# Optimization experiments

Measured on AMD Instinct MI355X. Metric: run time of the kernel, lower is better.

The kernel has to match this reference:

```python
import jax, jax.numpy as jnp
import numpy as np

N_NODES = 8192


def spmm(edge_src, edge_dst, edge_w, h):
    # out[dst] += w * h[src]  — sparse adjacency @ dense matrix
    msg = h[edge_src] * edge_w[:, None]
    return jax.ops.segment_sum(msg, edge_dst, num_segments=N_NODES)


def setup_inputs() -> dict:
    key = jax.random.key(0)
    k_x, k_s, k_d, k_w, k_w1, k_w2 = jax.random.split(key, 6)
    x = jax.random.normal(k_x, (N_NODES, 512), dtype=jnp.float32)
    edge_src = jax.random.randint(k_s, (262144,), 0, N_NODES, dtype=jnp.int32)
    edge_dst = jax.random.randint(k_d, (262144,), 0, N_NODES, dtype=jnp.int32)
    edge_w = jax.random.uniform(k_w, (262144,), dtype=jnp.float32)
    W1 = jax.random.normal(k_w1, (512, 256), dtype=jnp.float32) * 0.05
    W2 = jax.random.normal(k_w2, (256, 64), dtype=jnp.float32) * 0.05
    return {"x": x, "edge_src": edge_src, "edge_dst": edge_dst,
            "edge_w": edge_w, "W1": W1, "W2": W2}


def reference(x, edge_src, edge_dst, edge_w, W1, W2):
    # GCN layer 1: relu(A @ (X W1))
    h1 = jax.nn.relu(spmm(edge_src, edge_dst, edge_w, x @ W1))
    # GCN layer 2 (linear act): Z = A @ (H1 W2)
    z = spmm(edge_src, edge_dst, edge_w, h1 @ W2)
    # InnerProductDecoder with identity act: Z @ Z^T
    recon = jnp.einsum('nd,md->nm', z, z)
    return recon
```

## Files before the change

### kernel.cpp

```cpp
#include <hip/hip_runtime.h>
#include <hip/hip_bf16.h>

#define NN     8192
#define D0     512
#define D1     256
#define D2     64
#define NE     262144

typedef __attribute__((ext_vector_type(8)))  __bf16 bf16x8;
typedef __attribute__((ext_vector_type(16))) float  f32x16;

__global__ __launch_bounds__(256) void prep_k(const float* __restrict__ X,
                                              const float* __restrict__ W,
                                              int4* __restrict__ zero_region,
                                              __bf16* __restrict__ Xh,
                                              __bf16* __restrict__ Xl,
                                              __bf16* __restrict__ Th,
                                              __bf16* __restrict__ Tl) {
    const int bid = blockIdx.x;
    const int tid = threadIdx.x;
    if (bid < 16) {
        zero_region[bid * 256 + tid] = make_int4(0, 0, 0, 0);
    } else if (bid < 16 + 2048) {
        const int i = (bid - 16) * 256 + tid;
        float4 v0 = reinterpret_cast<const float4*>(X)[i * 2 + 0];
        float4 v1 = reinterpret_cast<const float4*>(X)[i * 2 + 1];
        float f[8] = {v0.x, v0.y, v0.z, v0.w, v1.x, v1.y, v1.z, v1.w};
        bf16x8 h, l;
        #pragma unroll
        for (int j = 0; j < 8; ++j) {
            __bf16 hj = (__bf16)f[j];
            h[j] = hj;
            l[j] = (__bf16)(f[j] - (float)hj);
        }
        reinterpret_cast<bf16x8*>(Xh)[i] = h;
        reinterpret_cast<bf16x8*>(Xl)[i] = l;
    } else {
        __shared__ float t[32][33];
        const int cid = bid - 16 - 2048;
        const int c0 = (cid & 7) * 32;
        const int k0 = (cid >> 3) * 32;
        {
            int tr  = tid >> 3;
            int tc4 = tid & 7;
            float4 v = *reinterpret_cast<const float4*>(&W[(k0 + tr) * D1 + c0 + tc4 * 4]);
            t[tr][tc4 * 4 + 0] = v.x;
            t[tr][tc4 * 4 + 1] = v.y;
            t[tr][tc4 * 4 + 2] = v.z;
            t[tr][tc4 * 4 + 3] = v.w;
        }
        __syncthreads();
        int c  = tid >> 3;
        int kq = (tid & 7) * 4;
        __bf16 hv[4], lv[4];
        #pragma unroll
        for (int j = 0; j < 4; ++j) {
            float f = t[kq + j][c];
            hv[j] = (__bf16)f;
            lv[j] = (__bf16)(f - (float)hv[j]);
        }
        *reinterpret_cast<uint2*>(&Th[(size_t)(c0 + c) * D0 + k0 + kq]) = *reinterpret_cast<uint2*>(hv);
        *reinterpret_cast<uint2*>(&Tl[(size_t)(c0 + c) * D0 + k0 + kq]) = *reinterpret_cast<uint2*>(lv);
    }
}

__global__ __launch_bounds__(256) void gemm1_mfma_k(const __bf16* __restrict__ Xh,
                                                    const __bf16* __restrict__ Xl,
                                                    const __bf16* __restrict__ Wh,
                                                    const __bf16* __restrict__ Wl,
                                                    float* __restrict__ O) {
    const int tid  = threadIdx.x;
    const int lane = tid & 63;
    const int w    = tid >> 6;
    const int wm   = w >> 1;
    const int wn   = w & 1;
    const int r32  = lane & 31;
    const int kh   = lane >> 5;
    const int row  = blockIdx.x * 64 + wm * 32 + r32;
    const int col  = blockIdx.y * 64 + wn * 32 + r32;

    const __bf16* pAh = Xh + (size_t)row * D0;
    const __bf16* pAl = Xl + (size_t)row * D0;
    const __bf16* pBh = Wh + (size_t)col * D0;
    const __bf16* pBl = Wl + (size_t)col * D0;

    f32x16 acc = {};
    #pragma unroll 8
    for (int k0 = 0; k0 < D0; k0 += 16) {
        const int koff = k0 + kh * 8;
        bf16x8 ah = *reinterpret_cast<const bf16x8*>(pAh + koff);
        bf16x8 al = *reinterpret_cast<const bf16x8*>(pAl + koff);
        bf16x8 bh = *reinterpret_cast<const bf16x8*>(pBh + koff);
        bf16x8 bl = *reinterpret_cast<const bf16x8*>(pBl + koff);
        acc = __builtin_amdgcn_mfma_f32_32x32x16_bf16(ah, bh, acc, 0, 0, 0);
        acc = __builtin_amdgcn_mfma_f32_32x32x16_bf16(ah, bl, acc, 0, 0, 0);
        acc = __builtin_amdgcn_mfma_f32_32x32x16_bf16(al, bh, acc, 0, 0, 0);
    }

    const int rowBase = blockIdx.x * 64 + wm * 32;
    const int colBase = blockIdx.y * 64 + wn * 32;
    #pragma unroll
    for (int reg = 0; reg < 16; ++reg) {
        int r = (reg & 3) + 8 * (reg >> 2) + 4 * kh;
        O[(size_t)(rowBase + r) * D1 + colBase + r32] = acc[reg];
    }
}

__global__ __launch_bounds__(256) void hist_k(const int* __restrict__ dst,
                                              int* __restrict__ counts) {
    int i = blockIdx.x * 256 + threadIdx.x;
    if (i < NE) atomicAdd(&counts[dst[i]], 1);
}

__global__ __launch_bounds__(256) void scan_k(const int* __restrict__ counts,
                                              int* __restrict__ rs) {
    __shared__ int wsum[4];
    const int tid  = threadIdx.x;
    const int base = tid * 32;
    int v[32];
    int s = 0;
    #pragma unroll
    for (int j = 0; j < 8; ++j) {
        int4 q = reinterpret_cast<const int4*>(&counts[base])[j];
        v[j * 4 + 0] = q.x; v[j * 4 + 1] = q.y; v[j * 4 + 2] = q.z; v[j * 4 + 3] = q.w;
        s += q.x + q.y + q.z + q.w;
    }
    int inc = s;
    #pragma unroll
    for (int off = 1; off < 64; off <<= 1) {
        int t = __shfl_up(inc, off, 64);
        if ((tid & 63) >= off) inc += t;
    }
    if ((tid & 63) == 63) wsum[tid >> 6] = inc;
    __syncthreads();
    int wpre = 0;
    #pragma unroll
    for (int wi = 0; wi < 4; ++wi) if (wi < (tid >> 6)) wpre += wsum[wi];
    int ex = wpre + inc - s;
    #pragma unroll
    for (int j = 0; j < 32; ++j) { rs[base + j] = ex; ex += v[j]; }
    if (tid == 0) rs[NN] = NE;
}

__global__ __launch_bounds__(256) void scatter_k(const int* __restrict__ src,
                                                 const int* __restrict__ dst,
                                                 const float* __restrict__ w,
                                                 const int* __restrict__ rs,
                                                 int* __restrict__ cursor,
                                                 int* __restrict__ eps,
                                                 float* __restrict__ epw) {
    int i = blockIdx.x * 256 + threadIdx.x;
    if (i < NE) {
        int d = dst[i];
        int pos = rs[d] + atomicAdd(&cursor[d], 1);
        eps[pos] = src[i];
        epw[pos] = w[i];
    }
}

__global__ __launch_bounds__(256) void spmmfuse_k(const float* __restrict__ Hin,
                                                  const int* __restrict__ rs,
                                                  const int* __restrict__ eps,
                                                  const float* __restrict__ epw,
                                                  const float* __restrict__ W2,
                                                  float* __restrict__ H1W2) {
    __shared__ float h1row[D1];
    const int row = blockIdx.x;
    const int tid = threadIdx.x;
    const int start = rs[row], end = rs[row + 1];
    float acc = 0.f;
    for (int j = start; j < end; ++j) {
        acc += epw[j] * Hin[(size_t)eps[j] * D1 + tid];
    }
    h1row[tid] = fmaxf(acc, 0.f);
    __syncthreads();
    if (tid < D2) {
        float o = 0.f;
        #pragma unroll 16
        for (int k = 0; k < D1; ++k) o += h1row[k] * W2[k * D2 + tid];
        H1W2[(size_t)row * D2 + tid] = o;
    }
}

__global__ __launch_bounds__(256) void spmm64_k(const float* __restrict__ Hin,
                                                const int* __restrict__ rs,
                                                const int* __restrict__ eps,
                                                const float* __restrict__ epw,
                                                __bf16* __restrict__ Zh,
                                                __bf16* __restrict__ Zl) {
    const int row = blockIdx.x * 4 + (threadIdx.x >> 6);
    const int c = threadIdx.x & 63;
    const int start = rs[row], end = rs[row + 1];
    float acc = 0.f;
    for (int j = start; j < end; ++j) {
        acc += epw[j] * Hin[eps[j] * D2 + c];
    }
    __bf16 h = (__bf16)acc;
    Zh[row * D2 + c] = h;
    Zl[row * D2 + c] = (__bf16)(acc - (float)h);
}

__global__ __launch_bounds__(256) void zzt_k(const __bf16* __restrict__ Zh,
                                             const __bf16* __restrict__ Zl,
                                             float* __restrict__ O) {
    const int tid  = threadIdx.x;
    const int lane = tid & 63;
    const int w    = tid >> 6;
    const int wm   = w >> 1;
    const int wn   = w & 1;
    const int r32  = lane & 31;
    const int kh   = lane >> 5;
    const int rowBase = blockIdx.y * 128 + wm * 64;
    const int colBase = blockIdx.x * 128 + wn * 64;

    f32x16 acc[2][2] = {};

    #pragma unroll
    for (int kk = 0; kk < 4; ++kk) {
        const int koff = kk * 16 + kh * 8;
        bf16x8 ah0 = *reinterpret_cast<const bf16x8*>(&Zh[(rowBase +      r32) * D2 + koff]);
        bf16x8 ah1 = *reinterpret_cast<const bf16x8*>(&Zh[(rowBase + 32 + r32) * D2 + koff]);
        bf16x8 al0 = *reinterpret_cast<const bf16x8*>(&Zl[(rowBase +      r32) * D2 + koff]);
        bf16x8 al1 = *reinterpret_cast<const bf16x8*>(&Zl[(rowBase + 32 + r32) * D2 + koff]);
        bf16x8 bh0 = *reinterpret_cast<const bf16x8*>(&Zh[(colBase +      r32) * D2 + koff]);
        bf16x8 bh1 = *reinterpret_cast<const bf16x8*>(&Zh[(colBase + 32 + r32) * D2 + koff]);
        bf16x8 bl0 = *reinterpret_cast<const bf16x8*>(&Zl[(colBase +      r32) * D2 + koff]);
        bf16x8 bl1 = *reinterpret_cast<const bf16x8*>(&Zl[(colBase + 32 + r32) * D2 + koff]);

        acc[0][0] = __builtin_amdgcn_mfma_f32_32x32x16_bf16(ah0, bh0, acc[0][0], 0, 0, 0);
        acc[0][1] = __builtin_amdgcn_mfma_f32_32x32x16_bf16(ah0, bh1, acc[0][1], 0, 0, 0);
        acc[1][0] = __builtin_amdgcn_mfma_f32_32x32x16_bf16(ah1, bh0, acc[1][0], 0, 0, 0);
        acc[1][1] = __builtin_amdgcn_mfma_f32_32x32x16_bf16(ah1, bh1, acc[1][1], 0, 0, 0);

        acc[0][0] = __builtin_amdgcn_mfma_f32_32x32x16_bf16(ah0, bl0, acc[0][0], 0, 0, 0);
        acc[0][1] = __builtin_amdgcn_mfma_f32_32x32x16_bf16(ah0, bl1, acc[0][1], 0, 0, 0);
        acc[1][0] = __builtin_amdgcn_mfma_f32_32x32x16_bf16(ah1, bl0, acc[1][0], 0, 0, 0);
        acc[1][1] = __builtin_amdgcn_mfma_f32_32x32x16_bf16(ah1, bl1, acc[1][1], 0, 0, 0);

        acc[0][0] = __builtin_amdgcn_mfma_f32_32x32x16_bf16(al0, bh0, acc[0][0], 0, 0, 0);
        acc[0][1] = __builtin_amdgcn_mfma_f32_32x32x16_bf16(al0, bh1, acc[0][1], 0, 0, 0);
        acc[1][0] = __builtin_amdgcn_mfma_f32_32x32x16_bf16(al1, bh0, acc[1][0], 0, 0, 0);
        acc[1][1] = __builtin_amdgcn_mfma_f32_32x32x16_bf16(al1, bh1, acc[1][1], 0, 0, 0);
    }

    #pragma unroll
    for (int i = 0; i < 2; ++i)
        #pragma unroll
        for (int j = 0; j < 2; ++j)
            #pragma unroll
            for (int reg = 0; reg < 16; ++reg) {
                int r = (reg & 3) + 8 * (reg >> 2) + 4 * kh;
                __builtin_nontemporal_store(acc[i][j][reg],
                    &O[(size_t)(rowBase + i * 32 + r) * NN + colBase + j * 32 + r32]);
            }
}

extern "C" void kernel_launch(void* const* d_in, const int* in_sizes, int n_in,
                              void* d_out, int out_size, void* d_ws, size_t ws_size,
                              hipStream_t stream) {
    const float* x        = (const float*)d_in[0];
    const int*   edge_src = (const int*)d_in[1];
    const int*   edge_dst = (const int*)d_in[2];
    const float* edge_w   = (const float*)d_in[3];
    const float* W1       = (const float*)d_in[4];
    const float* W2       = (const float*)d_in[5];
    float* out = (float*)d_out;

    char* ws = (char*)d_ws;
    const size_t OFF_XW1  = 0;
    const size_t OFF_H1W2 = OFF_XW1  + (size_t)NN * D1 * 4;
    const size_t OFF_ZH   = OFF_H1W2 + (size_t)NN * D2 * 4;
    const size_t OFF_ZL   = OFF_ZH   + (size_t)NN * D2 * 2;
    const size_t OFF_XH   = OFF_ZL   + (size_t)NN * D2 * 2;
    const size_t OFF_XL   = OFF_XH   + (size_t)NN * D0 * 2;
    const size_t OFF_WTH  = OFF_XL   + (size_t)NN * D0 * 2;
    const size_t OFF_WTL  = OFF_WTH  + (size_t)D0 * D1 * 2;
    const size_t OFF_RS   = OFF_WTL  + (size_t)D0 * D1 * 2;
    const size_t OFF_CNT  = OFF_RS   + 33280;
    const size_t OFF_CUR  = OFF_CNT  + (size_t)NN * 4;
    const size_t OFF_EPS  = OFF_CUR  + (size_t)NN * 4;
    const size_t OFF_EPW  = OFF_EPS  + (size_t)NE * 4;

    float*  xw1  = (float*)(ws + OFF_XW1);
    float*  h1w2 = (float*)(ws + OFF_H1W2);
    __bf16* zh   = (__bf16*)(ws + OFF_ZH);
    __bf16* zl   = (__bf16*)(ws + OFF_ZL);
    __bf16* xh   = (__bf16*)(ws + OFF_XH);
    __bf16* xl   = (__bf16*)(ws + OFF_XL);
    __bf16* wth  = (__bf16*)(ws + OFF_WTH);
    __bf16* wtl  = (__bf16*)(ws + OFF_WTL);
    int*    rs   = (int*)(ws + OFF_RS);
    int*    cnt  = (int*)(ws + OFF_CNT);
    int*    eps  = (int*)(ws + OFF_EPS);
    float*  epw  = (float*)(ws + OFF_EPW);
    int*    cur  = (int*)(ws + OFF_CUR);

    prep_k<<<16 + 2048 + 128, 256, 0, stream>>>(x, W1, (int4*)cnt, xh, xl, wth, wtl);

    gemm1_mfma_k<<<dim3(NN / 64, D1 / 64), 256, 0, stream>>>(xh, xl, wth, wtl, xw1);

    hist_k<<<NE / 256, 256, 0, stream>>>(edge_dst, cnt);
    scan_k<<<1, 256, 0, stream>>>(cnt, rs);
    scatter_k<<<NE / 256, 256, 0, stream>>>(edge_src, edge_dst, edge_w, rs, cur, eps, epw);

    spmmfuse_k<<<NN, 256, 0, stream>>>(xw1, rs, eps, epw, W2, h1w2);

    spmm64_k<<<NN / 4, 256, 0, stream>>>(h1w2, rs, eps, epw, zh, zl);

    zzt_k<<<dim3(NN / 128, NN / 128), 256, 0, stream>>>(zh, zl, out);
}
```

Measured before the change: 235.4 us.

## Exploit ZZ^T symmetry, fuse X bf16 split into GEMM1, batch SpMM rows

The Z·Z^T kernel now launches only the upper-triangular 128x128 tiles. Each off-diagonal tile writes its transpose through a padded shared-memory buffer, which roughly halves the MFMA work for the dominant output GEMM. The X hi/lo bf16 split moves from prep_k into a 128x128-tiled gemm1, removing a round trip of X through global memory. hist_k reads int4 destination indices, and spmmfuse_k handles four rows per block with W2 cached in shared memory. Costs include large shared-memory use (about 67 KB in zzt, 64 KB in spmmfuse) that lowers occupancy, and redundant per-k conversion work in gemm1.

```diff
diff --git a/kernel.cpp b/kernel.cpp
--- a/kernel.cpp
+++ b/kernel.cpp
@@ -9,35 +9,19 @@
 
 typedef __attribute__((ext_vector_type(8)))  __bf16 bf16x8;
 typedef __attribute__((ext_vector_type(16))) float  f32x16;
-
-__global__ __launch_bounds__(256) void prep_k(const float* __restrict__ X,
-                                              const float* __restrict__ W,
+typedef __attribute__((ext_vector_type(4)))  float  f32x4;
+
+__global__ __launch_bounds__(256) void prep_k(const float* __restrict__ W,
                                               int4* __restrict__ zero_region,
-                                              __bf16* __restrict__ Xh,
-                                              __bf16* __restrict__ Xl,
                                               __bf16* __restrict__ Th,
                                               __bf16* __restrict__ Tl) {
     const int bid = blockIdx.x;
     const int tid = threadIdx.x;
     if (bid < 16) {
         zero_region[bid * 256 + tid] = make_int4(0, 0, 0, 0);
-    } else if (bid < 16 + 2048) {
-        const int i = (bid - 16) * 256 + tid;
-        float4 v0 = reinterpret_cast<const float4*>(X)[i * 2 + 0];
-        float4 v1 = reinterpret_cast<const float4*>(X)[i * 2 + 1];
-        float f[8] = {v0.x, v0.y, v0.z, v0.w, v1.x, v1.y, v1.z, v1.w};
-        bf16x8 h, l;
-        #pragma unroll
-        for (int j = 0; j < 8; ++j) {
-            __bf16 hj = (__bf16)f[j];
-            h[j] = hj;
-            l[j] = (__bf16)(f[j] - (float)hj);
-        }
-        reinterpret_cast<bf16x8*>(Xh)[i] = h;
-        reinterpret_cast<bf16x8*>(Xl)[i] = l;
     } else {
         __shared__ float t[32][33];
-        const int cid = bid - 16 - 2048;
+        const int cid = bid - 16;
         const int c0 = (cid & 7) * 32;
         const int k0 = (cid >> 3) * 32;
         {
@@ -64,8 +48,7 @@
     }
 }
 
-__global__ __launch_bounds__(256) void gemm1_mfma_k(const __bf16* __restrict__ Xh,
-                                                    const __bf16* __restrict__ Xl,
+__global__ __launch_bounds__(256) void gemm1_mfma_k(const float* __restrict__ X,
                                                     const __bf16* __restrict__ Wh,
                                                     const __bf16* __restrict__ Wl,
                                                     float* __restrict__ O) {
@@ -76,40 +59,62 @@
     const int wn   = w & 1;
     const int r32  = lane & 31;
     const int kh   = lane >> 5;
-    const int row  = blockIdx.x * 64 + wm * 32 + r32;
-    const int col  = blockIdx.y * 64 + wn * 32 + r32;
-
-    const __bf16* pAh = Xh + (size_t)row * D0;
-    const __bf16* pAl = Xl + (size_t)row * D0;
-    const __bf16* pBh = Wh + (size_t)col * D0;
-    const __bf16* pBl = Wl + (size_t)col * D0;
-
-    f32x16 acc = {};
-    #pragma unroll 8
+    const int rowBase = blockIdx.x * 128 + wm * 64;
+    const int colBase = blockIdx.y * 128 + wn * 64;
+
+    f32x16 acc[2][2] = {};
+
     for (int k0 = 0; k0 < D0; k0 += 16) {
         const int koff = k0 + kh * 8;
-        bf16x8 ah = *reinterpret_cast<const bf16x8*>(pAh + koff);
-        bf16x8 al = *reinterpret_cast<const bf16x8*>(pAl + koff);
-        bf16x8 bh = *reinterpret_cast<const bf16x8*>(pBh + koff);
-        bf16x8 bl = *reinterpret_cast<const bf16x8*>(pBl + koff);
-        acc = __builtin_amdgcn_mfma_f32_32x32x16_bf16(ah, bh, acc, 0, 0, 0);
-        acc = __builtin_amdgcn_mfma_f32_32x32x16_bf16(ah, bl, acc, 0, 0, 0);
-        acc = __builtin_amdgcn_mfma_f32_32x32x16_bf16(al, bh, acc, 0, 0, 0);
-    }
-
-    const int rowBase = blockIdx.x * 64 + wm * 32;
-    const int colBase = blockIdx.y * 64 + wn * 32;
-    #pragma unroll
-    for (int reg = 0; reg < 16; ++reg) {
-        int r = (reg & 3) + 8 * (reg >> 2) + 4 * kh;
-        O[(size_t)(rowBase + r) * D1 + colBase + r32] = acc[reg];
-    }
-}
-
-__global__ __launch_bounds__(256) void hist_k(const int* __restrict__ dst,
+        bf16x8 ah[2], al[2];
+        #pragma unroll
+        for (int i = 0; i < 2; ++i) {
+            const float* px = X + (size_t)(rowBase + i * 32 + r32) * D0 + koff;
+            float4 f0 = *reinterpret_cast<const float4*>(px);
+            float4 f1 = *reinterpret_cast<const float4*>(px + 4);
+            float f[8] = {f0.x, f0.y, f0.z, f0.w, f1.x, f1.y, f1.z, f1.w};
+            #pragma unroll
+            for (int e = 0; e < 8; ++e) {
+                __bf16 hj = (__bf16)f[e];
+                ah[i][e] = hj;
+                al[i][e] = (__bf16)(f[e] - (float)hj);
+            }
+        }
+        bf16x8 bh[2], bl[2];
+        #pragma unroll
+        for (int j = 0; j < 2; ++j) {
+            bh[j] = *reinterpret_cast<const bf16x8*>(Wh + (size_t)(colBase + j * 32 + r32) * D0 + koff);
+            bl[j] = *reinterpret_cast<const bf16x8*>(Wl + (size_t)(colBase + j * 32 + r32) * D0 + koff);
+        }
+        #pragma unroll
+        for (int i = 0; i < 2; ++i)
+            #pragma unroll
+            for (int j = 0; j < 2; ++j) {
+                acc[i][j] = __builtin_amdgcn_mfma_f32_32x32x16_bf16(ah[i], bh[j], acc[i][j], 0, 0, 0);
+                acc[i][j] = __builtin_amdgcn_mfma_f32_32x32x16_bf16(ah[i], bl[j], acc[i][j], 0, 0, 0);
+                acc[i][j] = __builtin_amdgcn_mfma_f32_32x32x16_bf16(al[i], bh[j], acc[i][j], 0, 0, 0);
+            }
+    }
+
+    #pragma unroll
+    for (int i = 0; i < 2; ++i)
+        #pragma unroll
+        for (int j = 0; j < 2; ++j)
+            #pragma unroll
+            for (int reg = 0; reg < 16; ++reg) {
+                int r = (reg & 3) + 8 * (reg >> 2) + 4 * kh;
+                O[(size_t)(rowBase + i * 32 + r) * D1 + colBase + j * 32 + r32] = acc[i][j][reg];
+            }
+}
+
+__global__ __launch_bounds__(256) void hist_k(const int4* __restrict__ dst4,
                                               int* __restrict__ counts) {
     int i = blockIdx.x * 256 + threadIdx.x;
-    if (i < NE) atomicAdd(&counts[dst[i]], 1);
+    int4 d = dst4[i];
+    atomicAdd(&counts[d.x], 1);
+    atomicAdd(&counts[d.y], 1);
+    atomicAdd(&counts[d.z], 1);
+    atomicAdd(&counts[d.w], 1);
 }
 
 __global__ __launch_bounds__(256) void scan_k(const int* __restrict__ counts,
@@ -158,27 +163,42 @@
     }
 }
 
+#define SF_ROWS 4
 __global__ __launch_bounds__(256) void spmmfuse_k(const float* __restrict__ Hin,
                                                   const int* __restrict__ rs,
                                                   const int* __restrict__ eps,
                                                   const float* __restrict__ epw,
                                                   const float* __restrict__ W2,
                                                   float* __restrict__ H1W2) {
+    __shared__ float w2s[D1 * D2];
     __shared__ float h1row[D1];
-    const int row = blockIdx.x;
+    __shared__ float part[4][D2];
     const int tid = threadIdx.x;
-    const int start = rs[row], end = rs[row + 1];
-    float acc = 0.f;
-    for (int j = start; j < end; ++j) {
-        acc += epw[j] * Hin[(size_t)eps[j] * D1 + tid];
-    }
-    h1row[tid] = fmaxf(acc, 0.f);
-    __syncthreads();
-    if (tid < D2) {
+    #pragma unroll
+    for (int l = 0; l < 16; ++l) {
+        int idx = l * 256 + tid;
+        reinterpret_cast<float4*>(w2s)[idx] = reinterpret_cast<const float4*>(W2)[idx];
+    }
+    const int row0 = blockIdx.x * SF_ROWS;
+    const int c  = tid & 63;
+    const int ks = tid >> 6;
+    for (int rr = 0; rr < SF_ROWS; ++rr) {
+        const int row = row0 + rr;
+        const int start = rs[row], end = rs[row + 1];
+        float acc = 0.f;
+        for (int j = start; j < end; ++j) {
+            acc += epw[j] * Hin[(size_t)eps[j] * D1 + tid];
+        }
+        __syncthreads();
+        h1row[tid] = fmaxf(acc, 0.f);
+        __syncthreads();
         float o = 0.f;
-        #pragma unroll 16
-        for (int k = 0; k < D1; ++k) o += h1row[k] * W2[k * D2 + tid];
-        H1W2[(size_t)row * D2 + tid] = o;
+        #pragma unroll
+        for (int k = 0; k < 64; ++k) o += h1row[ks * 64 + k] * w2s[(ks * 64 + k) * D2 + c];
+        part[ks][c] = o;
+        __syncthreads();
+        if (tid < D2)
+            H1W2[(size_t)row * D2 + tid] = part[0][tid] + part[1][tid] + part[2][tid] + part[3][tid];
     }
 }
 
@@ -203,6 +223,15 @@
 __global__ __launch_bounds__(256) void zzt_k(const __bf16* __restrict__ Zh,
                                              const __bf16* __restrict__ Zl,
                                              float* __restrict__ O) {
+    __shared__ float tt[128][132];
+    const int bid = blockIdx.x;
+    int bx = (int)((sqrtf(8.f * bid + 1.f) - 1.f) * 0.5f);
+    while ((bx + 1) * (bx + 2) / 2 <= bid) ++bx;
+    while (bx * (bx + 1) / 2 > bid) --bx;
+    const int by = bid - bx * (bx + 1) / 2;
+    const int R = by * 128;
+    const int C = bx * 128;
+
     const int tid  = threadIdx.x;
     const int lane = tid & 63;
     const int w    = tid >> 6;
@@ -210,8 +239,8 @@
     const int wn   = w & 1;
     const int r32  = lane & 31;
     const int kh   = lane >> 5;
-    const int rowBase = blockIdx.y * 128 + wm * 64;
-    const int colBase = blockIdx.x * 128 + wn * 64;
+    const int rowBase = R + wm * 64;
+    const int colBase = C + wn * 64;
 
     f32x16 acc[2][2] = {};
 
@@ -251,8 +280,31 @@
             for (int reg = 0; reg < 16; ++reg) {
                 int r = (reg & 3) + 8 * (reg >> 2) + 4 * kh;
                 __builtin_nontemporal_store(acc[i][j][reg],
-                    &O[(size_t)(rowBase + i * 32 + r) * NN + colBase + j * 32 + r32]);
+                    &O[(size_t)(R + wm * 64 + i * 32 + r) * NN + C + wn * 64 + j * 32 + r32]);
             }
+
+    if (bx != by) {
+        #pragma unroll
+        for (int i = 0; i < 2; ++i)
+            #pragma unroll
+            for (int j = 0; j < 2; ++j)
+                #pragma unroll
+                for (int reg = 0; reg < 16; ++reg) {
+                    int r = wm * 64 + i * 32 + (reg & 3) + 8 * (reg >> 2) + 4 * kh;
+                    int cc = wn * 64 + j * 32 + r32;
+                    tt[cc][r] = acc[i][j][reg];
+                }
+        __syncthreads();
+        const int c    = tid >> 1;
+        const int half = tid & 1;
+        const float* srcp = &tt[c][half * 64];
+        float* dstp = &O[(size_t)(C + c) * NN + R + half * 64];
+        #pragma unroll
+        for (int m = 0; m < 16; ++m) {
+            f32x4 v = *reinterpret_cast<const f32x4*>(srcp + m * 4);
+            __builtin_nontemporal_store(v, reinterpret_cast<f32x4*>(dstp + m * 4));
+        }
+    }
 }
 
 extern "C" void kernel_launch(void* const* d_in, const int* in_sizes, int n_in,
@@ -271,9 +323,7 @@
     const size_t OFF_H1W2 = OFF_XW1  + (size_t)NN * D1 * 4;
     const size_t OFF_ZH   = OFF_H1W2 + (size_t)NN * D2 * 4;
     const size_t OFF_ZL   = OFF_ZH   + (size_t)NN * D2 * 2;
-    const size_t OFF_XH   = OFF_ZL   + (size_t)NN * D2 * 2;
-    const size_t OFF_XL   = OFF_XH   + (size_t)NN * D0 * 2;
-    const size_t OFF_WTH  = OFF_XL   + (size_t)NN * D0 * 2;
+    const size_t OFF_WTH  = OFF_ZL   + (size_t)NN * D2 * 2;
     const size_t OFF_WTL  = OFF_WTH  + (size_t)D0 * D1 * 2;
     const size_t OFF_RS   = OFF_WTL  + (size_t)D0 * D1 * 2;
     const size_t OFF_CNT  = OFF_RS   + 33280;
@@ -285,27 +335,25 @@
     float*  h1w2 = (float*)(ws + OFF_H1W2);
     __bf16* zh   = (__bf16*)(ws + OFF_ZH);
     __bf16* zl   = (__bf16*)(ws + OFF_ZL);
-    __bf16* xh   = (__bf16*)(ws + OFF_XH);
-    __bf16* xl   = (__bf16*)(ws + OFF_XL);
     __bf16* wth  = (__bf16*)(ws + OFF_WTH);
     __bf16* wtl  = (__bf16*)(ws + OFF_WTL);
     int*    rs   = (int*)(ws + OFF_RS);
     int*    cnt  = (int*)(ws + OFF_CNT);
+    int*    cur  = (int*)(ws + OFF_CUR);
     int*    eps  = (int*)(ws + OFF_EPS);
     float*  epw  = (float*)(ws + OFF_EPW);
-    int*    cur  = (int*)(ws + OFF_CUR);
-
-    prep_k<<<16 + 2048 + 128, 256, 0, stream>>>(x, W1, (int4*)cnt, xh, xl, wth, wtl);
-
-    gemm1_mfma_k<<<dim3(NN / 64, D1 / 64), 256, 0, stream>>>(xh, xl, wth, wtl, xw1);
-
-    hist_k<<<NE / 256, 256, 0, stream>>>(edge_dst, cnt);
+
+    prep_k<<<16 + 128, 256, 0, stream>>>(W1, (int4*)cnt, wth, wtl);
+
+    gemm1_mfma_k<<<dim3(NN / 128, D1 / 128), 256, 0, stream>>>(x, wth, wtl, xw1);
+
+    hist_k<<<NE / 4 / 256, 256, 0, stream>>>((const int4*)edge_dst, cnt);
     scan_k<<<1, 256, 0, stream>>>(cnt, rs);
     scatter_k<<<NE / 256, 256, 0, stream>>>(edge_src, edge_dst, edge_w, rs, cur, eps, epw);
 
-    spmmfuse_k<<<NN, 256, 0, stream>>>(xw1, rs, eps, epw, W2, h1w2);
+    spmmfuse_k<<<NN / SF_ROWS, 256, 0, stream>>>(xw1, rs, eps, epw, W2, h1w2);
 
     spmm64_k<<<NN / 4, 256, 0, stream>>>(h1w2, rs, eps, epw, zh, zl);
 
-    zzt_k<<<dim3(NN / 128, NN / 128), 256, 0, stream>>>(zh, zl, out);
-}
+    zzt_k<<<2080, 256, 0, stream>>>(zh, zl, out);
+}
```

Result: slower. 624.6 us (+165.4%).
